# Kernel tuning notes

Hardware: AMD Instinct MI355X
Metric: run time of the kernel (lower is better)

The kernel has to match this reference:

```python
import jax, jax.numpy as jnp
import numpy as np

H_G, W_G = 9, 25
N_NODES = H_G * W_G  # 225


def _grid_edge_index():
    # 8-connected grid graph INCLUDING self loops (di=dj=0), matching build_grid_edge_index.
    # PyG GATConv's remove_self_loops+add_self_loops leaves this edge set unchanged.
    edges = []
    for i in range(H_G):
        for j in range(W_G):
            nid = i * W_G + j
            for di in (-1, 0, 1):
                for dj in (-1, 0, 1):
                    ni, nj = i + di, j + dj
                    if 0 <= ni < H_G and 0 <= nj < W_G:
                        edges.append((nid, ni * W_G + nj))
    return jnp.asarray(np.array(edges, dtype=np.int32).T)  # [2, 1825]


def _gat(x, edge_index, W, a_src, a_dst, bias, concat):
    # x: [B, N, F_in]; W: [F_in, heads*d]; a_src/a_dst: [heads, d]
    B = x.shape[0]
    heads, d = a_src.shape
    h = (x @ W).reshape(B, N_NODES, heads, d)          # [B,N,H,D]
    src, dst = edge_index[0], edge_index[1]            # message flows src -> dst
    asrc = jnp.einsum('bnhd,hd->bnh', h, a_src)        # [B,N,H]
    adst = jnp.einsum('bnhd,hd->bnh', h, a_dst)
    e = jax.nn.leaky_relu(asrc[:, src] + adst[:, dst], 0.2)  # [B,E,H]
    et = jnp.transpose(e, (1, 0, 2))                   # [E,B,H] (segment ops over leading axis)
    m = jax.ops.segment_max(et, dst, num_segments=N_NODES)  # [N,B,H]
    ex = jnp.exp(et - m[dst])
    s = jax.ops.segment_sum(ex, dst, num_segments=N_NODES)
    alpha = ex / s[dst]                                # softmax over incoming edges per node
    ht = jnp.transpose(h, (1, 0, 2, 3))                # [N,B,H,D]
    out = jax.ops.segment_sum(alpha[..., None] * ht[src], dst, num_segments=N_NODES)  # [N,B,H,D]
    out = jnp.transpose(out, (1, 0, 2, 3))             # [B,N,H,D]
    if concat:
        out = out.reshape(B, N_NODES, heads * d)
    else:
        out = out.mean(axis=2)
    return out + bias


def setup_inputs() -> dict:
    key = jax.random.key(0)
    ks = jax.random.split(key, 16)
    B = 128
    s = 0.02
    inp = {
        'x4': jax.random.normal(ks[0], (B, 2048, 9, 25), dtype=jnp.float32),
        'pool_w': jax.random.normal(ks[1], (8, 2048), dtype=jnp.float32) * s,
        'pool_b': jnp.zeros((8,), dtype=jnp.float32),
        'gat1_w': jax.random.normal(ks[2], (8, 64), dtype=jnp.float32) * s,
        'gat1_asrc': jax.random.normal(ks[3], (4, 16), dtype=jnp.float32) * s,
        'gat1_adst': jax.random.normal(ks[4], (4, 16), dtype=jnp.float32) * s,
        'gat1_b': jnp.zeros((64,), dtype=jnp.float32),
        'gat2_w': jax.random.normal(ks[5], (64, 8), dtype=jnp.float32) * s,
        'gat2_asrc': jax.random.normal(ks[6], (1, 8), dtype=jnp.float32) * s,
        'gat2_adst': jax.random.normal(ks[7], (1, 8), dtype=jnp.float32) * s,
        'gat2_b': jnp.zeros((8,), dtype=jnp.float32),
        'w1': jax.random.normal(ks[8], (1800, 2048), dtype=jnp.float32) * 0.01,
        'b1': jnp.zeros((2048,), dtype=jnp.float32),
        'w2': jax.random.normal(ks[9], (2048, 20800), dtype=jnp.float32) * 0.01,
        'b2': jnp.zeros((20800,), dtype=jnp.float32),
        'edge_index': _grid_edge_index(),
    }
    return inp


def reference(x4, pool_w, pool_b, gat1_w, gat1_asrc, gat1_adst, gat1_b,
              gat2_w, gat2_asrc, gat2_adst, gat2_b, w1, b1, w2, b2, edge_index):
    B = x4.shape[0]
    # 1x1 conv pool: 2048 -> 8 channels (already 9x25, adaptive_avg_pool2d is identity)
    fea = jnp.einsum('bchw,oc->bohw', x4, pool_w) + pool_b[None, :, None, None]
    fea = fea.reshape(B, 8, N_NODES).transpose(0, 2, 1)  # [B, 225, 8]
    x1 = jax.nn.relu(_gat(fea, edge_index, gat1_w, gat1_asrc, gat1_adst, gat1_b, concat=True))
    x2 = _gat(x1, edge_index, gat2_w, gat2_asrc, gat2_adst, gat2_b, concat=False)  # [B,225,8]
    flat = x2.reshape(B, -1)                             # [B, 1800]
    hid = jax.nn.relu(flat @ w1 + b1)
    out = hid @ w2 + b2
    return out.reshape(-1, 100, 52, 4)
```

## Files before the change

### kernel.cpp

```cpp
#include <hip/hip_runtime.h>
#include <hip/hip_bf16.h>


typedef __attribute__((ext_vector_type(8))) short bh8_t;
typedef __attribute__((ext_vector_type(4))) float f32x4;

static __device__ __forceinline__ short f2bs(float f) {
    __hip_bfloat16 h = __float2bfloat16(f);
    return *reinterpret_cast<short*>(&h);
}
static __device__ __forceinline__ unsigned pack2(short a, short b) {
    return (unsigned)(unsigned short)a | ((unsigned)(unsigned short)b << 16);
}

__global__ __launch_bounds__(256) void pool_kernel(const float* __restrict__ x4,
                                                   const float* __restrict__ pool_w,
                                                   float* __restrict__ part) {
    const int b  = blockIdx.x >> 3;
    const int ch = blockIdx.x & 7;
    const int tid = threadIdx.x;
    if (tid >= 225) return;
    const float* xp = x4 + ((size_t)b * 2048 + (size_t)ch * 256) * 225 + tid;
    const float* wp = pool_w + ch * 256;
    float a[8] = {};
#pragma unroll 8
    for (int c = 0; c < 256; ++c) {
        const float v = xp[c * 225];
#pragma unroll
        for (int o = 0; o < 8; ++o) a[o] += v * wp[o * 2048 + c];
    }
    float* dst = part + (size_t)b * 14400 + ch * 1800 + tid * 8;
    *reinterpret_cast<float4*>(dst)     = make_float4(a[0], a[1], a[2], a[3]);
    *reinterpret_cast<float4*>(dst + 4) = make_float4(a[4], a[5], a[6], a[7]);
}

__global__ __launch_bounds__(256) void gat_kernel(const float* __restrict__ part,
                                                  const float* __restrict__ pool_b,
                                                  const float* __restrict__ w1g,
                                                  const float* __restrict__ a1src,
                                                  const float* __restrict__ a1dst,
                                                  const float* __restrict__ b1g,
                                                  const float* __restrict__ w2g,
                                                  const float* __restrict__ a2src,
                                                  const float* __restrict__ a2dst,
                                                  const float* __restrict__ b2g,
                                                  short* __restrict__ flat) {
    __shared__ __align__(16) float att[1800];
    __shared__ __align__(16) float h[14400];
    const int b = blockIdx.x;
    const int tid = threadIdx.x;

    for (int i = tid; i < 1800; i += 256) {
        const float* p = part + (size_t)b * 14400 + i;
        float s = 0;
#pragma unroll
        for (int c = 0; c < 8; ++c) s += p[c * 1800];
        att[i] = s + pool_b[i & 7];
    }
    __syncthreads();

    {
        const int o = tid & 63, mr = tid >> 6;
        float wv[8];
#pragma unroll
        for (int k = 0; k < 8; ++k) wv[k] = w1g[k * 64 + o];
        for (int n = mr; n < 225; n += 4) {
            float acc = 0;
#pragma unroll
            for (int k = 0; k < 8; ++k) acc += att[n * 8 + k] * wv[k];
            h[n * 64 + o] = acc;
        }
    }
    __syncthreads();

    for (int t = tid; t < 900; t += 256) {
        const int n = t >> 2, hd = t & 3;
        const float* hp = &h[n * 64 + hd * 16];
        float as = 0, ad = 0;
#pragma unroll
        for (int d = 0; d < 16; ++d) {
            float hv = hp[d];
            as += hv * a1src[hd * 16 + d];
            ad += hv * a1dst[hd * 16 + d];
        }
        att[t] = as;
        att[900 + t] = ad;
    }
    __syncthreads();

    float o1[4][16];
#pragma unroll
    for (int r = 0; r < 4; ++r) {
        const int task = tid + 256 * r;
        if (task < 900) {
            const int n = task >> 2, hd = task & 3;
            const int i = n / 25, j = n % 25;
            const float adn = att[900 + task];
            float e[9];
            int sid[9];
            float mx = -1e30f;
#pragma unroll
            for (int t9 = 0; t9 < 9; ++t9) {
                const int di = t9 / 3 - 1, dj = t9 % 3 - 1;
                const int ni = i + di, nj = j + dj;
                const bool valid = ((unsigned)ni < 9u) && ((unsigned)nj < 25u);
                const int s = valid ? ni * 25 + nj : n;
                sid[t9] = s;
                float ev = att[s * 4 + hd] + adn;
                ev = ev >= 0.f ? ev : 0.2f * ev;
                e[t9] = valid ? ev : -1e30f;
                mx = fmaxf(mx, e[t9]);
            }
            float sum = 0;
#pragma unroll
            for (int t9 = 0; t9 < 9; ++t9) {
                float ex = __expf(e[t9] - mx);
                e[t9] = ex;
                sum += ex;
            }
            const float inv = 1.f / sum;
            float out[16] = {};
#pragma unroll
            for (int t9 = 0; t9 < 9; ++t9) {
                const float al = e[t9] * inv;
                const float* hp = &h[sid[t9] * 64 + hd * 16];
#pragma unroll
                for (int d = 0; d < 16; ++d) out[d] += al * hp[d];
            }
            const float* bp = b1g + hd * 16;
#pragma unroll
            for (int d = 0; d < 16; ++d) o1[r][d] = fmaxf(out[d] + bp[d], 0.f);
        }
    }
    __syncthreads();

#pragma unroll
    for (int r = 0; r < 4; ++r) {
        const int task = tid + 256 * r;
        if (task < 900) {
            const int n = task >> 2, hd = task & 3;
#pragma unroll
            for (int d = 0; d < 16; ++d) h[n * 64 + hd * 16 + d] = o1[r][d];
        }
    }
    __syncthreads();

    if (tid < 225) {
        const int n = tid;
        float acc8[8] = {};
#pragma unroll 4
        for (int k = 0; k < 64; k += 4) {
            const float4 xv = *reinterpret_cast<const float4*>(&h[n * 64 + k]);
#pragma unroll
            for (int o = 0; o < 8; ++o) {
                acc8[o] += xv.x * w2g[k * 8 + o] + xv.y * w2g[(k + 1) * 8 + o]
                         + xv.z * w2g[(k + 2) * 8 + o] + xv.w * w2g[(k + 3) * 8 + o];
            }
        }
#pragma unroll
        for (int o = 0; o < 8; ++o) att[n * 8 + o] = acc8[o];
    }
    __syncthreads();

    if (tid < 225) {
        const int n = tid, i = n / 25, j = n % 25;
        float av[8], dv[8];
#pragma unroll
        for (int d = 0; d < 8; ++d) { av[d] = a2src[d]; dv[d] = a2dst[d]; }
        float adn = 0;
#pragma unroll
        for (int d = 0; d < 8; ++d) adn += att[n * 8 + d] * dv[d];
        float e[9];
        int sid[9];
        float mx = -1e30f;
#pragma unroll
        for (int t9 = 0; t9 < 9; ++t9) {
            const int di = t9 / 3 - 1, dj = t9 % 3 - 1;
            const int ni = i + di, nj = j + dj;
            const bool valid = ((unsigned)ni < 9u) && ((unsigned)nj < 25u);
            const int s = valid ? ni * 25 + nj : n;
            sid[t9] = s;
            float as = 0;
#pragma unroll
            for (int d = 0; d < 8; ++d) as += att[s * 8 + d] * av[d];
            float ev = as + adn;
            ev = ev >= 0.f ? ev : 0.2f * ev;
            e[t9] = valid ? ev : -1e30f;
            mx = fmaxf(mx, e[t9]);
        }
        float sum = 0;
#pragma unroll
        for (int t9 = 0; t9 < 9; ++t9) {
            float ex = __expf(e[t9] - mx);
            e[t9] = ex;
            sum += ex;
        }
        const float inv = 1.f / sum;
        float out[8] = {};
#pragma unroll
        for (int t9 = 0; t9 < 9; ++t9) {
            const float al = e[t9] * inv;
            const float* hp = &att[sid[t9] * 8];
#pragma unroll
            for (int d = 0; d < 8; ++d) out[d] += al * hp[d];
        }
        short* dst = flat + (size_t)b * 1824 + n * 8;
#pragma unroll
        for (int d = 0; d < 8; ++d) dst[d] = f2bs(out[d] + b2g[d]);
    }
    if (tid < 24) flat[(size_t)b * 1824 + 1800 + tid] = 0;
}

template <int BN, int MT, int NT, int NWN, bool RELU, bool OUT_BF16>
__global__ __launch_bounds__(256) void gemm_mfma(const short* __restrict__ A,
                                                 const float* __restrict__ Wf,
                                                 const float* __restrict__ bias,
                                                 void* __restrict__ outp,
                                                 int K, int Kw, int N) {
    constexpr int LDT = 40;
    __shared__ __align__(16) short sA[2][128 * LDT];
    __shared__ __align__(16) short sB[2][BN * LDT];
    const int tid = threadIdx.x;
    const int lane = tid & 63;
    const int wave = tid >> 6;
    const int n0 = blockIdx.x * BN;
    const int wm0 = (wave / NWN) * (MT * 16);
    const int wn0 = (wave % NWN) * (NT * 16);
    const int lm = lane & 15;
    const int lkb = (lane >> 4) * 8;

    const int am = tid >> 1;
    const int akh = tid & 1;
    constexpr int EPT = (32 * BN) / 256;
    const int bn_ = tid % BN;
    const int bk0 = (tid / BN) * EPT;

    f32x4 acc[MT][NT] = {};
    const int nkt = K >> 5;

    uint4 va0, va1;
    float bv[EPT];

    auto LOAD = [&](int kt) {
        const int k0 = kt << 5;
        const uint4* src = reinterpret_cast<const uint4*>(A + (size_t)am * K + k0 + akh * 16);
        va0 = src[0];
        va1 = src[1];
#pragma unroll
        for (int jj = 0; jj < EPT; ++jj) {
            int kk = k0 + bk0 + jj;
            if (kk >= Kw) kk = Kw - 1;
            bv[jj] = Wf[(size_t)kk * N + n0 + bn_];
        }
    };
    auto STORE = [&](int buf) {
        uint4* dstA = reinterpret_cast<uint4*>(&sA[buf][am * LDT + akh * 16]);
        dstA[0] = va0;
        dstA[1] = va1;
        unsigned uw[EPT / 2];
#pragma unroll
        for (int jj = 0; jj < EPT / 2; ++jj)
            uw[jj] = pack2(f2bs(bv[2 * jj]), f2bs(bv[2 * jj + 1]));
        if constexpr (EPT == 8) {
            uint4 u;
            u.x = uw[0]; u.y = uw[1]; u.z = uw[2]; u.w = uw[3];
            *reinterpret_cast<uint4*>(&sB[buf][bn_ * LDT + bk0]) = u;
        } else {
            *reinterpret_cast<unsigned*>(&sB[buf][bn_ * LDT + bk0]) = uw[0];
        }
    };

    LOAD(0);
    STORE(0);
    __syncthreads();

    int cur = 0;
    for (int kt = 0; kt < nkt; ++kt) {
        const bool more = (kt + 1 < nkt);
        if (more) LOAD(kt + 1);
        bh8_t bfr[NT];
#pragma unroll
        for (int nt = 0; nt < NT; ++nt)
            bfr[nt] = *reinterpret_cast<const bh8_t*>(&sB[cur][(wn0 + nt * 16 + lm) * LDT + lkb]);
#pragma unroll
        for (int mt = 0; mt < MT; ++mt) {
            bh8_t afr = *reinterpret_cast<const bh8_t*>(&sA[cur][(wm0 + mt * 16 + lm) * LDT + lkb]);
#pragma unroll
            for (int nt = 0; nt < NT; ++nt)
                acc[mt][nt] = __builtin_amdgcn_mfma_f32_16x16x32_bf16(afr, bfr[nt], acc[mt][nt], 0, 0, 0);
        }
        if (more) STORE(cur ^ 1);
        __syncthreads();
        cur ^= 1;
    }

    const int rg = lane >> 4;
#pragma unroll
    for (int nt = 0; nt < NT; ++nt) {
        const int n = n0 + wn0 + nt * 16 + lm;
        const float bvv = bias[n];
#pragma unroll
        for (int mt = 0; mt < MT; ++mt) {
#pragma unroll
            for (int r = 0; r < 4; ++r) {
                const int m = wm0 + mt * 16 + rg * 4 + r;
                float v = acc[mt][nt][r] + bvv;
                if (RELU) v = fmaxf(v, 0.f);
                if (OUT_BF16)
                    reinterpret_cast<short*>(outp)[(size_t)m * N + n] = f2bs(v);
                else
                    reinterpret_cast<float*>(outp)[(size_t)m * N + n] = v;
            }
        }
    }
}

extern "C" void kernel_launch(void* const* d_in, const int* in_sizes, int n_in,
                              void* d_out, int out_size, void* d_ws, size_t ws_size,
                              hipStream_t stream) {
    const float* x4        = (const float*)d_in[0];
    const float* pool_w    = (const float*)d_in[1];
    const float* pool_b    = (const float*)d_in[2];
    const float* gat1_w    = (const float*)d_in[3];
    const float* gat1_asrc = (const float*)d_in[4];
    const float* gat1_adst = (const float*)d_in[5];
    const float* gat1_b    = (const float*)d_in[6];
    const float* gat2_w    = (const float*)d_in[7];
    const float* gat2_asrc = (const float*)d_in[8];
    const float* gat2_adst = (const float*)d_in[9];
    const float* gat2_b    = (const float*)d_in[10];
    const float* w1        = (const float*)d_in[11];
    const float* b1        = (const float*)d_in[12];
    const float* w2        = (const float*)d_in[13];
    const float* b2        = (const float*)d_in[14];
    float* out = (float*)d_out;

    char* ws = (char*)d_ws;
    float* part = (float*)ws;
    short* flat = (short*)(ws + 7372800);
    short* hid  = (short*)(ws + 7372800 + 466944);

    pool_kernel<<<1024, 256, 0, stream>>>(x4, pool_w, part);
    gat_kernel<<<128, 256, 0, stream>>>(part, pool_b, gat1_w, gat1_asrc, gat1_adst, gat1_b,
                                        gat2_w, gat2_asrc, gat2_adst, gat2_b, flat);
    gemm_mfma<16, 2, 1, 1, true, true><<<128, 256, 0, stream>>>(flat, w1, b1, (void*)hid, 1824, 1800, 2048);
    gemm_mfma<64, 4, 2, 2, false, false><<<325, 256, 0, stream>>>(hid, w2, b2, (void*)out, 2048, 2048, 20800);
}
```

Measured before the change: 546.8 us.

## Swizzle GAT shared-memory layout and deepen GEMM global prefetch by one stage

Result: faster. 533.5 us (-2.4%).

```diff
diff --git a/kernel.cpp b/kernel.cpp
--- a/kernel.cpp
+++ b/kernel.cpp
@@ -11,6 +11,9 @@
 }
 static __device__ __forceinline__ unsigned pack2(short a, short b) {
     return (unsigned)(unsigned short)a | ((unsigned)(unsigned short)b << 16);
+}
+static __device__ __forceinline__ int hsw(int n, int g) {
+    return n * 64 + ((g ^ (n & 15)) << 2);
 }
 
 __global__ __launch_bounds__(256) void pool_kernel(const float* __restrict__ x4,
@@ -61,6 +64,7 @@
 
     {
         const int o = tid & 63, mr = tid >> 6;
+        const int g = o >> 2, e = o & 3;
         float wv[8];
 #pragma unroll
         for (int k = 0; k < 8; ++k) wv[k] = w1g[k * 64 + o];
@@ -68,23 +72,29 @@
             float acc = 0;
 #pragma unroll
             for (int k = 0; k < 8; ++k) acc += att[n * 8 + k] * wv[k];
-            h[n * 64 + o] = acc;
-        }
-    }
-    __syncthreads();
-
-    for (int t = tid; t < 900; t += 256) {
-        const int n = t >> 2, hd = t & 3;
-        const float* hp = &h[n * 64 + hd * 16];
-        float as = 0, ad = 0;
-#pragma unroll
-        for (int d = 0; d < 16; ++d) {
-            float hv = hp[d];
-            as += hv * a1src[hd * 16 + d];
-            ad += hv * a1dst[hd * 16 + d];
-        }
-        att[t] = as;
-        att[900 + t] = ad;
+            h[hsw(n, g) + e] = acc;
+        }
+    }
+    __syncthreads();
+
+    float adnr[4];
+#pragma unroll
+    for (int r = 0; r < 4; ++r) {
+        const int t = tid + 256 * r;
+        if (t < 900) {
+            const int n = t >> 2, hd = t & 3;
+            float as = 0, ad = 0;
+#pragma unroll
+            for (int q = 0; q < 4; ++q) {
+                const float4 hv = *reinterpret_cast<const float4*>(&h[hsw(n, hd * 4 + q)]);
+                const float* s4 = &a1src[hd * 16 + q * 4];
+                const float* d4 = &a1dst[hd * 16 + q * 4];
+                as += hv.x * s4[0] + hv.y * s4[1] + hv.z * s4[2] + hv.w * s4[3];
+                ad += hv.x * d4[0] + hv.y * d4[1] + hv.z * d4[2] + hv.w * d4[3];
+            }
+            att[t] = as;
+            adnr[r] = ad;
+        }
     }
     __syncthreads();
 
@@ -95,7 +105,7 @@
         if (task < 900) {
             const int n = task >> 2, hd = task & 3;
             const int i = n / 25, j = n % 25;
-            const float adn = att[900 + task];
+            const float adn = adnr[r];
             float e[9];
             int sid[9];
             float mx = -1e30f;
@@ -123,9 +133,15 @@
 #pragma unroll
             for (int t9 = 0; t9 < 9; ++t9) {
                 const float al = e[t9] * inv;
-                const float* hp = &h[sid[t9] * 64 + hd * 16];
-#pragma unroll
-                for (int d = 0; d < 16; ++d) out[d] += al * hp[d];
+                const int s = sid[t9];
+#pragma unroll
+                for (int q = 0; q < 4; ++q) {
+                    const float4 hv = *reinterpret_cast<const float4*>(&h[hsw(s, hd * 4 + q)]);
+                    out[q * 4 + 0] += al * hv.x;
+                    out[q * 4 + 1] += al * hv.y;
+                    out[q * 4 + 2] += al * hv.z;
+                    out[q * 4 + 3] += al * hv.w;
+                }
             }
             const float* bp = b1g + hd * 16;
 #pragma unroll
@@ -140,7 +156,10 @@
         if (task < 900) {
             const int n = task >> 2, hd = task & 3;
 #pragma unroll
-            for (int d = 0; d < 16; ++d) h[n * 64 + hd * 16 + d] = o1[r][d];
+            for (int q = 0; q < 4; ++q)
+                *reinterpret_cast<float4*>(&h[hsw(n, hd * 4 + q)]) =
+                    make_float4(o1[r][q * 4 + 0], o1[r][q * 4 + 1],
+                                o1[r][q * 4 + 2], o1[r][q * 4 + 3]);
         }
     }
     __syncthreads();
@@ -148,9 +167,10 @@
     if (tid < 225) {
         const int n = tid;
         float acc8[8] = {};
-#pragma unroll 4
-        for (int k = 0; k < 64; k += 4) {
-            const float4 xv = *reinterpret_cast<const float4*>(&h[n * 64 + k]);
+#pragma unroll
+        for (int g = 0; g < 16; ++g) {
+            const float4 xv = *reinterpret_cast<const float4*>(&h[hsw(n, g)]);
+            const int k = g * 4;
 #pragma unroll
             for (int o = 0; o < 8; ++o) {
                 acc8[o] += xv.x * w2g[k * 8 + o] + xv.y * w2g[(k + 1) * 8 + o]
@@ -158,7 +178,7 @@
             }
         }
 #pragma unroll
-        for (int o = 0; o < 8; ++o) att[n * 8 + o] = acc8[o];
+        for (int o = 0; o < 8; ++o) att[o * 225 + n] = acc8[o];
     }
     __syncthreads();
 
@@ -169,7 +189,7 @@
         for (int d = 0; d < 8; ++d) { av[d] = a2src[d]; dv[d] = a2dst[d]; }
         float adn = 0;
 #pragma unroll
-        for (int d = 0; d < 8; ++d) adn += att[n * 8 + d] * dv[d];
+        for (int d = 0; d < 8; ++d) adn += att[d * 225 + n] * dv[d];
         float e[9];
         int sid[9];
         float mx = -1e30f;
@@ -182,7 +202,7 @@
             sid[t9] = s;
             float as = 0;
 #pragma unroll
-            for (int d = 0; d < 8; ++d) as += att[s * 8 + d] * av[d];
+            for (int d = 0; d < 8; ++d) as += att[d * 225 + s] * av[d];
             float ev = as + adn;
             ev = ev >= 0.f ? ev : 0.2f * ev;
             e[t9] = valid ? ev : -1e30f;
@@ -200,9 +220,9 @@
 #pragma unroll
         for (int t9 = 0; t9 < 9; ++t9) {
             const float al = e[t9] * inv;
-            const float* hp = &att[sid[t9] * 8];
-#pragma unroll
-            for (int d = 0; d < 8; ++d) out[d] += al * hp[d];
+            const int s = sid[t9];
+#pragma unroll
+            for (int d = 0; d < 8; ++d) out[d] += al * att[d * 225 + s];
         }
         short* dst = flat + (size_t)b * 1824 + n * 8;
 #pragma unroll
@@ -272,12 +292,11 @@
 
     LOAD(0);
     STORE(0);
+    if (nkt > 1) LOAD(1);
     __syncthreads();
 
     int cur = 0;
     for (int kt = 0; kt < nkt; ++kt) {
-        const bool more = (kt + 1 < nkt);
-        if (more) LOAD(kt + 1);
         bh8_t bfr[NT];
 #pragma unroll
         for (int nt = 0; nt < NT; ++nt)
@@ -289,7 +308,8 @@
             for (int nt = 0; nt < NT; ++nt)
                 acc[mt][nt] = __builtin_amdgcn_mfma_f32_16x16x32_bf16(afr, bfr[nt], acc[mt][nt], 0, 0, 0);
         }
-        if (more) STORE(cur ^ 1);
+        if (kt + 1 < nkt) STORE(cur ^ 1);
+        if (kt + 2 < nkt) LOAD(kt + 2);
         __syncthreads();
         cur ^= 1;
     }
```
